# Performance work log

Hardware: AMD Instinct MI355X
Metric: run time of the kernel (lower is better)

The kernel has to match this reference:

```python
import jax, jax.numpy as jnp
import numpy as np
import math

N, C, H = 2048, 256, 8
D = C // H
T, R, E = 8, 12, 32768
BUCKETS = 21
SEED = 128


def _layernorm(x, g, b, eps=1e-5):
    mu = jnp.mean(x, axis=-1, keepdims=True)
    var = jnp.var(x, axis=-1, keepdims=True)
    return (x - mu) * jax.lax.rsqrt(var + eps) * g + b


def _bucketize_dt(dt, num_buckets):
    eps = 1e-06
    signed_log = jnp.sign(dt) * jnp.log1p(jnp.abs(dt) + eps)
    min_v, max_v = -5.0, 5.0
    norm = (jnp.clip(signed_log, min_v, max_v) - min_v) / (max_v - min_v + 1e-09)
    idx = jnp.floor(norm * (num_buckets - 1)).astype(jnp.int32)
    return jnp.clip(idx, 0, num_buckets - 1)


def setup_inputs() -> dict:
    key = jax.random.key(0)
    ks = jax.random.split(key, 24)
    s = 0.02
    inp = {
        'X': jax.random.normal(ks[0], (N, C), jnp.float32),
        'token_type': jax.random.randint(ks[1], (N,), 0, T, jnp.int32),
        'edge_src': jax.random.randint(ks[2], (E,), 0, N, jnp.int32),
        'edge_dst': jax.random.randint(ks[3], (E,), 0, N, jnp.int32),
        'edge_rel': jax.random.randint(ks[4], (E,), 0, R, jnp.int32),
        'time_vec': jax.random.normal(ks[5], (N,), jnp.float32),
        'seed_count': SEED,
        'Wq': jax.random.normal(ks[6], (C, C), jnp.float32) * s,
        'bq': jnp.zeros((C,), jnp.float32),
        'Wk': jax.random.normal(ks[7], (C, C), jnp.float32) * s,
        'bk': jnp.zeros((C,), jnp.float32),
        'Wv': jax.random.normal(ks[8], (C, C), jnp.float32) * s,
        'bv': jnp.zeros((C,), jnp.float32),
        'Wo': jax.random.normal(ks[9], (C, C), jnp.float32) * s,
        'bo': jnp.zeros((C,), jnp.float32),
        'ln1_g': jnp.ones((C,), jnp.float32),
        'ln1_b': jnp.zeros((C,), jnp.float32),
        'ln2_g': jnp.ones((C,), jnp.float32),
        'ln2_b': jnp.zeros((C,), jnp.float32),
        'W1': jax.random.normal(ks[10], (C, 4 * C), jnp.float32) * s,
        'b1': jnp.zeros((4 * C,), jnp.float32),
        'W2': jax.random.normal(ks[11], (4 * C, C), jnp.float32) * s,
        'b2': jnp.zeros((C,), jnp.float32),
        'adj_rel_bias': jnp.zeros((R, H), jnp.float32),
        'typepair_bias': jnp.zeros((T, T, H), jnp.float32),
        'temp_bias': jax.random.normal(ks[12], (BUCKETS, H), jnp.float32) * s,
    }
    return inp


def reference(X, token_type, edge_src, edge_dst, edge_rel, time_vec, seed_count,
              Wq, bq, Wk, bk, Wv, bv, Wo, bo,
              ln1_g, ln1_b, ln2_g, ln2_b, W1, b1, W2, b2,
              adj_rel_bias, typepair_bias, temp_bias):
    n = X.shape[0]
    h = _layernorm(X, ln1_g, ln1_b)
    q = (h @ Wq + bq).reshape(n, H, D)
    k = (h @ Wk + bk).reshape(n, H, D)
    v = (h @ Wv + bv).reshape(n, H, D)
    scores = jnp.einsum('nhd,mhd->hnm', q, k) / math.sqrt(D)  # [H, N, N]

    # structural bias, factored as [N, N, H] then transposed
    bias = typepair_bias[token_type][:, token_type]            # [N, N, H]
    bias = bias.at[edge_src, edge_dst].add(adj_rel_bias[edge_rel])
    # seed-wise temporal bias on the first seed_count rows
    dt = time_vec[None, :] - time_vec[:seed_count, None]       # [S, N]
    tb = temp_bias[_bucketize_dt(dt, BUCKETS)]                 # [S, N, H]
    bias = bias.at[:seed_count].add(tb)

    attn = jax.nn.softmax(scores + bias.transpose(2, 0, 1), axis=-1)
    o = jnp.einsum('hnm,mhd->nhd', attn, v).reshape(n, C)
    x = X + (o @ Wo + bo)

    h2 = _layernorm(x, ln2_g, ln2_b)
    f = jax.nn.gelu(h2 @ W1 + b1, approximate=False) @ W2 + b2
    return x + f
```

## Files before the change

### kernel.cpp

```cpp
#include <hip/hip_runtime.h>
#include <hip/hip_bf16.h>
#include <math.h>

#define NTOK 2048
#define CDIM 256
#define HHEADS 8
#define DHEAD 32
#define NEDGE 32768
#define EXTD 64
#define LE 72

typedef __attribute__((ext_vector_type(8))) short short8;
typedef __attribute__((ext_vector_type(4))) short short4v;
typedef __attribute__((ext_vector_type(4))) float f32x4;

static __device__ inline short f2bf(float f) {
    __hip_bfloat16 h = __float2bfloat16(f);
    return *reinterpret_cast<short*>(&h);
}
static __device__ inline float bf2f(short s) {
    unsigned int u = ((unsigned int)(unsigned short)s) << 16;
    return *reinterpret_cast<float*>(&u);
}

__global__ __launch_bounds__(256) void ln4_kernel(const float* __restrict__ X,
    const float* __restrict__ g, const float* __restrict__ b, short* __restrict__ out)
{
    int t = threadIdx.x;
    int wv = t >> 6, lane = t & 63;
    int row = blockIdx.x * 4 + wv;

    float4 x = *(const float4*)&X[(size_t)row * CDIM + lane * 4];
    float s = x.x + x.y + x.z + x.w;
    #pragma unroll
    for (int off = 1; off < 64; off <<= 1) s += __shfl_xor(s, off);
    float mu = s * (1.0f / CDIM);
    float4 d = { x.x - mu, x.y - mu, x.z - mu, x.w - mu };
    float s2 = d.x * d.x + d.y * d.y + d.z * d.z + d.w * d.w;
    #pragma unroll
    for (int off = 1; off < 64; off <<= 1) s2 += __shfl_xor(s2, off);
    float rsig = rsqrtf(s2 * (1.0f / CDIM) + 1e-5f);
    float4 gg = *(const float4*)&g[lane * 4];
    float4 bb = *(const float4*)&b[lane * 4];
    short o4[4];
    o4[0] = f2bf(d.x * rsig * gg.x + bb.x);
    o4[1] = f2bf(d.y * rsig * gg.y + bb.y);
    o4[2] = f2bf(d.z * rsig * gg.z + bb.z);
    o4[3] = f2bf(d.w * rsig * gg.w + bb.w);
    *(short4v*)&out[(size_t)row * CDIM + lane * 4] = *(short4v*)o4;
}

static __device__ inline void transpose_tile_f32(const float* __restrict__ in,
    short* __restrict__ out, int K, int N, int k0, int n0, int t)
{
    __shared__ float tile[64][65];
    int r0 = t >> 4, c0 = (t & 15) * 4;
    #pragma unroll
    for (int i = 0; i < 4; i++) {
        int r = r0 + i * 16;
        float4 v = *(const float4*)(in + (size_t)(k0 + r) * N + n0 + c0);
        tile[r][c0 + 0] = v.x; tile[r][c0 + 1] = v.y;
        tile[r][c0 + 2] = v.z; tile[r][c0 + 3] = v.w;
    }
    __syncthreads();
    #pragma unroll
    for (int i = 0; i < 4; i++) {
        int nr = r0 + i * 16;
        short o4[4];
        #pragma unroll
        for (int j = 0; j < 4; j++) o4[j] = f2bf(tile[c0 + j][nr]);
        *(short4v*)(out + (size_t)(n0 + nr) * K + k0 + c0) = *(short4v*)o4;
    }
}

__global__ __launch_bounds__(256) void prep_kernel(
    const float* __restrict__ Wq, const float* __restrict__ Wk,
    const float* __restrict__ Wv, const float* __restrict__ Wo,
    const float* __restrict__ W1, const float* __restrict__ W2,
    short* __restrict__ wt_qkv, short* __restrict__ wot,
    short* __restrict__ w1t, short* __restrict__ w2t,
    const int* __restrict__ token_type, const float* __restrict__ typepair_bias,
    short* __restrict__ qh, short* __restrict__ kh,
    int* __restrict__ cnt)
{
    int b = blockIdx.x;
    int t = threadIdx.x;
    if (b < 192) {
        const float* src; short* dst; int K, N, bx, by;
        if (b < 64) {
            int m = b >> 4, r = b & 15;
            src = (m == 0) ? Wq : (m == 1) ? Wk : (m == 2) ? Wv : Wo;
            dst = (m == 0) ? wt_qkv : (m == 1) ? wt_qkv + 256 * 256
                : (m == 2) ? wt_qkv + 512 * 256 : wot;
            K = 256; N = 256; bx = r & 3; by = r >> 2;
        } else if (b < 128) {
            int r = b - 64; src = W1; dst = w1t; K = 256; N = 1024; bx = r & 15; by = r >> 4;
        } else {
            int r = b - 128; src = W2; dst = w2t; K = 1024; N = 256; bx = r & 3; by = r >> 2;
        }
        transpose_tile_f32(src, dst, K, N, by * 64, bx * 64, t);
    } else if (b < 256) {
        int idx = (b - 192) * 256 + t;
        int row = idx >> 3, h = idx & 7;
        int tt = token_type[row];
        short qe[32], ke[32];
        #pragma unroll
        for (int j = 0; j < 32; j++) {
            if (j < 8) {
                qe[j] = f2bf(typepair_bias[(tt * 8 + j) * 8 + h]);
                ke[j] = (j == tt) ? (short)0x3F80 : (short)0;
            } else { qe[j] = 0; ke[j] = 0; }
        }
        size_t base = ((size_t)h * NTOK + row) * EXTD + 32;
        #pragma unroll
        for (int k = 0; k < 4; k++) {
            *(short8*)&qh[base + k * 8] = *(short8*)&qe[k * 8];
            *(short8*)&kh[base + k * 8] = *(short8*)&ke[k * 8];
        }
    } else {
        #pragma unroll
        for (int i = 0; i < 8; i++) cnt[t * 8 + i] = 0;
    }
}

template<int EPI>
__global__ __launch_bounds__(256) void gemm32_kernel(
    const short* __restrict__ A, const short* __restrict__ Bt,
    const float* __restrict__ bias, const float* __restrict__ resid,
    void* __restrict__ out_, int M, int N, int K)
{
    __shared__ short A_lds[32 * 40];
    __shared__ short B_lds[64 * 40];

    const int t = threadIdx.x;
    const int w = t >> 6, lane = t & 63, c = lane & 15, g = lane >> 4;
    const int row0 = blockIdx.y * 32, col0 = blockIdx.x * 64;
    const int srow = t >> 2, sk = (t & 3) * 8;

    f32x4 acc[2] = {};

    for (int k0 = 0; k0 < K; k0 += 32) {
        if (t < 128)
            *(short8*)&A_lds[srow * 40 + sk] = *(const short8*)&A[(size_t)(row0 + srow) * K + k0 + sk];
        *(short8*)&B_lds[srow * 40 + sk] = *(const short8*)&Bt[(size_t)(col0 + srow) * K + k0 + sk];
        __syncthreads();
        short8 af = *(const short8*)&A_lds[((w & 1) * 16 + c) * 40 + g * 8];
        #pragma unroll
        for (int nf = 0; nf < 2; nf++) {
            short8 bf = *(const short8*)&B_lds[((w >> 1) * 32 + nf * 16 + c) * 40 + g * 8];
            acc[nf] = __builtin_amdgcn_mfma_f32_16x16x32_bf16(af, bf, acc[nf], 0, 0, 0);
        }
        __syncthreads();
    }

    #pragma unroll
    for (int nf = 0; nf < 2; nf++) {
        #pragma unroll
        for (int reg = 0; reg < 4; reg++) {
            int row = row0 + (w & 1) * 16 + g * 4 + reg;
            int col = col0 + (w >> 1) * 32 + nf * 16 + c;
            float v = acc[nf][reg] + bias[col];
            if (EPI == 2) {
                ((float*)out_)[(size_t)row * N + col] = v + resid[(size_t)row * N + col];
            } else {
                v = 0.5f * v * (1.0f + erff(v * 0.70710678118654752f));
                ((short*)out_)[(size_t)row * N + col] = f2bf(v);
            }
        }
    }
}

__global__ __launch_bounds__(256) void gemm32_qkv_kernel(
    const short* __restrict__ A, const short* __restrict__ Bt,
    const float* __restrict__ bq, const float* __restrict__ bk, const float* __restrict__ bv,
    short* __restrict__ qh, short* __restrict__ kh, short* __restrict__ vt)
{
    const int K = CDIM;
    __shared__ short A_lds[32 * 40];
    __shared__ short B_lds[64 * 40];

    const int t = threadIdx.x;
    const int w = t >> 6, lane = t & 63, c = lane & 15, g = lane >> 4;
    const int row0 = blockIdx.y * 32, col0 = blockIdx.x * 64;
    const int srow = t >> 2, sk = (t & 3) * 8;

    f32x4 acc[2] = {};

    for (int k0 = 0; k0 < K; k0 += 32) {
        if (t < 128)
            *(short8*)&A_lds[srow * 40 + sk] = *(const short8*)&A[(size_t)(row0 + srow) * K + k0 + sk];
        *(short8*)&B_lds[srow * 40 + sk] = *(const short8*)&Bt[(size_t)(col0 + srow) * K + k0 + sk];
        __syncthreads();
        short8 af = *(const short8*)&A_lds[((w & 1) * 16 + c) * 40 + g * 8];
        #pragma unroll
        for (int nf = 0; nf < 2; nf++) {
            short8 bf = *(const short8*)&B_lds[((w >> 1) * 32 + nf * 16 + c) * 40 + g * 8];
            acc[nf] = __builtin_amdgcn_mfma_f32_16x16x32_bf16(af, bf, acc[nf], 0, 0, 0);
        }
        __syncthreads();
    }

    const int region = col0 >> 8;
    const int colr0 = col0 & 255;
    const float* bias = (region == 0) ? bq : (region == 1) ? bk : bv;
    #pragma unroll
    for (int nf = 0; nf < 2; nf++) {
        #pragma unroll
        for (int reg = 0; reg < 4; reg++) {
            int row = row0 + (w & 1) * 16 + g * 4 + reg;
            int col = colr0 + (w >> 1) * 32 + nf * 16 + c;
            float v = acc[nf][reg] + bias[col];
            if (region == 0) v *= 0.17677669529663687f;
            short bb = f2bf(v);
            size_t hidx = ((size_t)(col >> 5) * NTOK + row) * EXTD + (col & 31);
            if (region == 0)      qh[hidx] = bb;
            else if (region == 1) kh[hidx] = bb;
            else                  vt[(size_t)col * NTOK + row] = bb;
        }
    }
}

__global__ void edge_hist_kernel(const int* __restrict__ src, int* __restrict__ cnt, int E)
{
    int e = blockIdx.x * blockDim.x + threadIdx.x;
    if (e < E) atomicAdd(&cnt[src[e]], 1);
}

__global__ __launch_bounds__(256) void edge_scan_kernel(const int* __restrict__ cnt,
    int* __restrict__ row_ptr, int* __restrict__ wcur)
{
    __shared__ int sums[256];
    int t = threadIdx.x;
    int base = t * 8;
    int local[8];
    int s = 0;
    #pragma unroll
    for (int i = 0; i < 8; i++) { local[i] = s; s += cnt[base + i]; }
    sums[t] = s;
    __syncthreads();
    for (int off = 1; off < 256; off <<= 1) {
        int v = (t >= off) ? sums[t - off] : 0;
        __syncthreads();
        sums[t] += v;
        __syncthreads();
    }
    int excl = (t == 0) ? 0 : sums[t - 1];
    #pragma unroll
    for (int i = 0; i < 8; i++) {
        int r = excl + local[i];
        row_ptr[base + i] = r;
        wcur[base + i] = r;
    }
    if (t == 255) row_ptr[NTOK] = sums[255];
}

__global__ void edge_scatter_kernel(const int* __restrict__ src, const int* __restrict__ dst,
    const int* __restrict__ rel, int* __restrict__ wcur, int2* __restrict__ pairs, int E)
{
    int e = blockIdx.x * blockDim.x + threadIdx.x;
    if (e < E) {
        int pos = atomicAdd(&wcur[src[e]], 1);
        pairs[pos] = make_int2(dst[e], rel[e]);
    }
}

__global__ __launch_bounds__(256) void sgemm_kernel(
    const short* __restrict__ qh, const short* __restrict__ kh,
    short* __restrict__ S)
{
    __shared__ short A_lds[64 * LE];
    __shared__ short B_lds[64 * LE];
    const int t = threadIdx.x;
    const int w = t >> 6, lane = t & 63, c = lane & 15, g = lane >> 4;
    const int h = blockIdx.z;
    const int m0 = blockIdx.x * 64, n0 = blockIdx.y * 64;

    {
        int r = t >> 3, off = (t & 7) * 8;
        *(short8*)&A_lds[r * LE + off] =
            *(const short8*)&qh[((size_t)h * NTOK + n0 + r) * EXTD + off];
        *(short8*)&A_lds[(r + 32) * LE + off] =
            *(const short8*)&qh[((size_t)h * NTOK + n0 + 32 + r) * EXTD + off];
        *(short8*)&B_lds[r * LE + off] =
            *(const short8*)&kh[((size_t)h * NTOK + m0 + r) * EXTD + off];
        *(short8*)&B_lds[(r + 32) * LE + off] =
            *(const short8*)&kh[((size_t)h * NTOK + m0 + 32 + r) * EXTD + off];
    }
    __syncthreads();

    short8 alo = *(const short8*)&A_lds[(w * 16 + c) * LE + g * 8];
    short8 ahi = *(const short8*)&A_lds[(w * 16 + c) * LE + 32 + g * 8];
    f32x4 acc[4] = {};
    #pragma unroll
    for (int nf = 0; nf < 4; nf++) {
        short8 blo = *(const short8*)&B_lds[(nf * 16 + c) * LE + g * 8];
        short8 bhi = *(const short8*)&B_lds[(nf * 16 + c) * LE + 32 + g * 8];
        acc[nf] = __builtin_amdgcn_mfma_f32_16x16x32_bf16(alo, blo, acc[nf], 0, 0, 0);
        acc[nf] = __builtin_amdgcn_mfma_f32_16x16x32_bf16(ahi, bhi, acc[nf], 0, 0, 0);
    }

    #pragma unroll
    for (int nf = 0; nf < 4; nf++)
        #pragma unroll
        for (int reg = 0; reg < 4; reg++) {
            int row = n0 + w * 16 + g * 4 + reg;
            int col = m0 + nf * 16 + c;
            S[((size_t)h * NTOK + row) * NTOK + col] = f2bf(acc[nf][reg]);
        }
}

__global__ __launch_bounds__(256) void softmax_kernel(
    short* __restrict__ S,
    const float* __restrict__ time_vec, const int* __restrict__ seed_ptr,
    const float* __restrict__ adj_rel_bias, const float* __restrict__ temp_bias,
    const int* __restrict__ row_ptr, const int2* __restrict__ pairs)
{
    int t = threadIdx.x, wv = t >> 6, lane = t & 63;
    int task = blockIdx.x * 4 + wv;
    int h = task >> 11, n = task & 2047;
    int seed = seed_ptr[0];
    bool temporal = (n < seed);
    float tn = time_vec[n];
    short* Srow = &S[((size_t)h * NTOK + n) * NTOK];

    float vv[32];
    #pragma unroll
    for (int i = 0; i < 4; i++) {
        int m0 = i * 512 + lane * 8;
        short8 sv = *(const short8*)&Srow[m0];
        float v[8];
        #pragma unroll
        for (int j = 0; j < 8; j++) v[j] = bf2f(sv[j]);
        if (temporal) {
            float4 ta = *(const float4*)&time_vec[m0];
            float4 tb = *(const float4*)&time_vec[m0 + 4];
            float tv8[8] = { ta.x, ta.y, ta.z, ta.w, tb.x, tb.y, tb.z, tb.w };
            #pragma unroll
            for (int j = 0; j < 8; j++) {
                float dt = tv8[j] - tn;
                float ab = fabsf(dt) + 1e-6f;
                float sg = (dt > 0.0f) ? 1.0f : ((dt < 0.0f) ? -1.0f : 0.0f);
                float sl = sg * log1pf(ab);
                sl = fminf(fmaxf(sl, -5.0f), 5.0f);
                float norm = (sl + 5.0f) * (1.0f / (10.0f + 1e-9f));
                int bidx = (int)floorf(norm * 20.0f);
                bidx = min(max(bidx, 0), 20);
                v[j] += temp_bias[bidx * 8 + h];
            }
        }
        #pragma unroll
        for (int j = 0; j < 8; j++) vv[i * 8 + j] = v[j];
    }

    {
        int e0 = row_ptr[n], e1 = row_ptr[n + 1];
        for (int e = e0; e < e1; ++e) {
            int2 pr = pairs[e];
            int col = pr.x;
            if (((col >> 3) & 63) == lane) {
                float ab = adj_rel_bias[pr.y * 8 + h];
                int ci = col >> 9;
                int sl = col & 7;
                #pragma unroll
                for (int q = 0; q < 4; q++) {
                    if (q == ci) {
                        #pragma unroll
                        for (int j = 0; j < 8; j++)
                            vv[q * 8 + j] += (j == sl) ? ab : 0.0f;
                    }
                }
            }
        }
    }

    float mx = vv[0];
    #pragma unroll
    for (int i = 1; i < 32; i++) mx = fmaxf(mx, vv[i]);
    #pragma unroll
    for (int off = 1; off < 64; off <<= 1) mx = fmaxf(mx, __shfl_xor(mx, off));
    float sum = 0.0f;
    #pragma unroll
    for (int i = 0; i < 32; i++) { vv[i] = __expf(vv[i] - mx); sum += vv[i]; }
    #pragma unroll
    for (int off = 1; off < 64; off <<= 1) sum += __shfl_xor(sum, off);
    float inv = 1.0f / sum;

    #pragma unroll
    for (int i = 0; i < 4; i++) {
        short p8[8];
        #pragma unroll
        for (int j = 0; j < 8; j++) p8[j] = f2bf(vv[i * 8 + j] * inv);
        *(short8*)&Srow[i * 512 + lane * 8] = *(short8*)p8;
    }
}

__global__ __launch_bounds__(256) void pv_kernel(
    const short* __restrict__ P, const short* __restrict__ vt,
    short* __restrict__ o)
{
    __shared__ short A_lds[32 * LE];
    __shared__ short B_lds[32 * LE];
    const int t = threadIdx.x;
    const int w = t >> 6, lane = t & 63, c = lane & 15, g = lane >> 4;
    const int h = blockIdx.y;
    const int n0 = blockIdx.x * 32;
    const int rowblk = (w & 1) * 16, colblk = (w >> 1) * 16;

    f32x4 acc = {0.0f, 0.0f, 0.0f, 0.0f};

    for (int k0 = 0; k0 < NTOK; k0 += 64) {
        int r = t >> 3, off = (t & 7) * 8;
        *(short8*)&A_lds[r * LE + off] =
            *(const short8*)&P[((size_t)h * NTOK + n0 + r) * NTOK + k0 + off];
        *(short8*)&B_lds[r * LE + off] =
            *(const short8*)&vt[(size_t)(h * 32 + r) * NTOK + k0 + off];
        __syncthreads();
        short8 alo = *(const short8*)&A_lds[(rowblk + c) * LE + g * 8];
        short8 ahi = *(const short8*)&A_lds[(rowblk + c) * LE + 32 + g * 8];
        short8 blo = *(const short8*)&B_lds[(colblk + c) * LE + g * 8];
        short8 bhi = *(const short8*)&B_lds[(colblk + c) * LE + 32 + g * 8];
        acc = __builtin_amdgcn_mfma_f32_16x16x32_bf16(alo, blo, acc, 0, 0, 0);
        acc = __builtin_amdgcn_mfma_f32_16x16x32_bf16(ahi, bhi, acc, 0, 0, 0);
        __syncthreads();
    }

    #pragma unroll
    for (int reg = 0; reg < 4; reg++) {
        int row = n0 + rowblk + g * 4 + reg;
        int col = h * 32 + colblk + c;
        o[(size_t)row * CDIM + col] = f2bf(acc[reg]);
    }
}

extern "C" void kernel_launch(void* const* d_in, const int* in_sizes, int n_in,
                              void* d_out, int out_size, void* d_ws, size_t ws_size,
                              hipStream_t stream)
{
    (void)in_sizes; (void)n_in; (void)out_size; (void)ws_size;
    const float* X        = (const float*)d_in[0];
    const int* token_type = (const int*)d_in[1];
    const int* edge_src   = (const int*)d_in[2];
    const int* edge_dst   = (const int*)d_in[3];
    const int* edge_rel   = (const int*)d_in[4];
    const float* time_vec = (const float*)d_in[5];
    const int* seed_ptr   = (const int*)d_in[6];
    const float* Wq = (const float*)d_in[7];  const float* bq = (const float*)d_in[8];
    const float* Wk = (const float*)d_in[9];  const float* bk = (const float*)d_in[10];
    const float* Wv = (const float*)d_in[11]; const float* bv = (const float*)d_in[12];
    const float* Wo = (const float*)d_in[13]; const float* bo = (const float*)d_in[14];
    const float* ln1_g = (const float*)d_in[15]; const float* ln1_b = (const float*)d_in[16];
    const float* ln2_g = (const float*)d_in[17]; const float* ln2_b = (const float*)d_in[18];
    const float* W1 = (const float*)d_in[19]; const float* b1 = (const float*)d_in[20];
    const float* W2 = (const float*)d_in[21]; const float* b2 = (const float*)d_in[22];
    const float* adj_rel_bias  = (const float*)d_in[23];
    const float* typepair_bias = (const float*)d_in[24];
    const float* temp_bias     = (const float*)d_in[25];
    float* out = (float*)d_out;

    char* base = (char*)d_ws;
    size_t off = 0;
    auto alloc = [&](size_t bytes) { char* p = base + off; off += (bytes + 255) & ~(size_t)255; return p; };
    short* qh_bf   = (short*)alloc((size_t)HHEADS * NTOK * EXTD * 2);
    short* kh_bf   = (short*)alloc((size_t)HHEADS * NTOK * EXTD * 2);
    short* vt_bf   = (short*)alloc((size_t)256 * NTOK * 2);
    short* h1_bf   = (short*)alloc((size_t)NTOK * 256 * 2);
    short* h2_bf   = (short*)alloc((size_t)NTOK * 256 * 2);
    short* o_bf    = (short*)alloc((size_t)NTOK * 256 * 2);
    short* mid_bf  = (short*)alloc((size_t)NTOK * 1024 * 2);
    float* xb      = (float*)alloc((size_t)NTOK * 256 * 4);
    short* wt_qkv  = (short*)alloc((size_t)768 * 256 * 2);
    short* wot     = (short*)alloc((size_t)256 * 256 * 2);
    short* w1t     = (short*)alloc((size_t)1024 * 256 * 2);
    short* w2t     = (short*)alloc((size_t)256 * 1024 * 2);
    int2*  pairs   = (int2*)alloc((size_t)NEDGE * 8);
    int*   cnt     = (int*)alloc((size_t)NTOK * 4);
    int*   rowptr  = (int*)alloc(((size_t)NTOK + 1) * 4);
    int*   wcur    = (int*)alloc((size_t)NTOK * 4);
    short* S       = (short*)alloc((size_t)HHEADS * NTOK * NTOK * 2);

    prep_kernel<<<257, 256, 0, stream>>>(Wq, Wk, Wv, Wo, W1, W2,
                                         wt_qkv, wot, w1t, w2t,
                                         token_type, typepair_bias,
                                         qh_bf, kh_bf, cnt);

    edge_hist_kernel<<<NEDGE / 256, 256, 0, stream>>>(edge_src, cnt, NEDGE);
    edge_scan_kernel<<<1, 256, 0, stream>>>(cnt, rowptr, wcur);
    edge_scatter_kernel<<<NEDGE / 256, 256, 0, stream>>>(edge_src, edge_dst, edge_rel, wcur, pairs, NEDGE);

    ln4_kernel<<<NTOK / 4, 256, 0, stream>>>(X, ln1_g, ln1_b, h1_bf);

    gemm32_qkv_kernel<<<dim3(12, 64), 256, 0, stream>>>(h1_bf, wt_qkv, bq, bk, bv,
                                                        qh_bf, kh_bf, vt_bf);

    sgemm_kernel<<<dim3(32, 32, 8), 256, 0, stream>>>(qh_bf, kh_bf, S);
    softmax_kernel<<<NTOK * HHEADS / 4, 256, 0, stream>>>(
        S, time_vec, seed_ptr, adj_rel_bias, temp_bias, rowptr, pairs);
    pv_kernel<<<dim3(64, 8), 256, 0, stream>>>(S, vt_bf, o_bf);

    gemm32_kernel<2><<<dim3(4, 64), 256, 0, stream>>>(o_bf, wot, bo, X, xb, NTOK, 256, 256);

    ln4_kernel<<<NTOK / 4, 256, 0, stream>>>(xb, ln2_g, ln2_b, h2_bf);

    gemm32_kernel<3><<<dim3(16, 64), 256, 0, stream>>>(h2_bf, w1t, b1, nullptr, mid_bf, NTOK, 1024, 256);
    gemm32_kernel<2><<<dim3(4, 64), 256, 0, stream>>>(mid_bf, w2t, b2, xb, out, NTOK, 256, 1024);
}
```

Before: 155.5 us.

## Fuse bias and unnormalized exp into score GEMM, defer softmax normalization to PV

Folds the separate softmax pass into the QK^T GEMM epilogue: edge, temporal and type biases are added there, exp is taken without a max subtraction, and row sums are accumulated with atomics. Normalization moves into the PV epilogue. The edge CSR is rebuilt keyed by (row, 64-column tile) so each GEMM tile reads only its own edges. This removes a full read and write of the H×N×N score matrix, but it drops the max subtraction, which risks overflow for large scores, and adds atomic contention on the row sums.

```diff
diff --git a/kernel.cpp b/kernel.cpp
--- a/kernel.cpp
+++ b/kernel.cpp
@@ -7,6 +7,7 @@
 #define HHEADS 8
 #define DHEAD 32
 #define NEDGE 32768
+#define NTILE2 32
 #define EXTD 64
 #define LE 72
 
@@ -81,7 +82,7 @@
     short* __restrict__ w1t, short* __restrict__ w2t,
     const int* __restrict__ token_type, const float* __restrict__ typepair_bias,
     short* __restrict__ qh, short* __restrict__ kh,
-    int* __restrict__ cnt)
+    int* __restrict__ cnt2, float* __restrict__ rowsum)
 {
     int b = blockIdx.x;
     int t = threadIdx.x;
@@ -117,9 +118,14 @@
             *(short8*)&qh[base + k * 8] = *(short8*)&qe[k * 8];
             *(short8*)&kh[base + k * 8] = *(short8*)&ke[k * 8];
         }
+    } else if (b < 288) {
+        int base = (b - 256) * 2048 + t * 8;
+        #pragma unroll
+        for (int i = 0; i < 8; i++) cnt2[base + i] = 0;
     } else {
-        #pragma unroll
-        for (int i = 0; i < 8; i++) cnt[t * 8 + i] = 0;
+        int base = (b - 288) * 2048 + t * 8;
+        #pragma unroll
+        for (int i = 0; i < 8; i++) rowsum[base + i] = 0.0f;
     }
 }
 
@@ -220,22 +226,21 @@
     }
 }
 
-__global__ void edge_hist_kernel(const int* __restrict__ src, int* __restrict__ cnt, int E)
+__global__ void edge_hist2_kernel(const int* __restrict__ src, const int* __restrict__ dst,
+    int* __restrict__ cnt, int E)
 {
     int e = blockIdx.x * blockDim.x + threadIdx.x;
-    if (e < E) atomicAdd(&cnt[src[e]], 1);
-}
-
-__global__ __launch_bounds__(256) void edge_scan_kernel(const int* __restrict__ cnt,
+    if (e < E) atomicAdd(&cnt[src[e] * NTILE2 + (dst[e] >> 6)], 1);
+}
+
+__global__ __launch_bounds__(256) void edge_scan2_kernel(const int* __restrict__ cnt,
     int* __restrict__ row_ptr, int* __restrict__ wcur)
 {
     __shared__ int sums[256];
     int t = threadIdx.x;
-    int base = t * 8;
-    int local[8];
+    int base = t * 256;
     int s = 0;
-    #pragma unroll
-    for (int i = 0; i < 8; i++) { local[i] = s; s += cnt[base + i]; }
+    for (int i = 0; i < 256; i++) s += cnt[base + i];
     sums[t] = s;
     __syncthreads();
     for (int off = 1; off < 256; off <<= 1) {
@@ -244,36 +249,44 @@
         sums[t] += v;
         __syncthreads();
     }
-    int excl = (t == 0) ? 0 : sums[t - 1];
-    #pragma unroll
-    for (int i = 0; i < 8; i++) {
-        int r = excl + local[i];
-        row_ptr[base + i] = r;
-        wcur[base + i] = r;
-    }
-    if (t == 255) row_ptr[NTOK] = sums[255];
-}
-
-__global__ void edge_scatter_kernel(const int* __restrict__ src, const int* __restrict__ dst,
+    int run = (t == 0) ? 0 : sums[t - 1];
+    for (int i = 0; i < 256; i++) {
+        row_ptr[base + i] = run;
+        wcur[base + i] = run;
+        run += cnt[base + i];
+    }
+    if (t == 255) row_ptr[NTOK * NTILE2] = run;
+}
+
+__global__ void edge_scatter2_kernel(const int* __restrict__ src, const int* __restrict__ dst,
     const int* __restrict__ rel, int* __restrict__ wcur, int2* __restrict__ pairs, int E)
 {
     int e = blockIdx.x * blockDim.x + threadIdx.x;
     if (e < E) {
-        int pos = atomicAdd(&wcur[src[e]], 1);
-        pairs[pos] = make_int2(dst[e], rel[e]);
-    }
-}
-
-__global__ __launch_bounds__(256) void sgemm_kernel(
+        int d = dst[e];
+        int pos = atomicAdd(&wcur[src[e] * NTILE2 + (d >> 6)], 1);
+        pairs[pos] = make_int2(d, rel[e]);
+    }
+}
+
+__global__ __launch_bounds__(256) void sgemm_exp_kernel(
     const short* __restrict__ qh, const short* __restrict__ kh,
-    short* __restrict__ S)
+    const float* __restrict__ time_vec, const int* __restrict__ seed_ptr,
+    const float* __restrict__ adj_rel_bias, const float* __restrict__ temp_bias,
+    const int* __restrict__ row_ptr2, const int2* __restrict__ pairs2,
+    short* __restrict__ S, float* __restrict__ rowsum)
 {
     __shared__ short A_lds[64 * LE];
     __shared__ short B_lds[64 * LE];
+    __shared__ float tcol_s[64];
+    __shared__ float temp_h[21];
+    __shared__ float adj_h[12];
+
     const int t = threadIdx.x;
     const int w = t >> 6, lane = t & 63, c = lane & 15, g = lane >> 4;
     const int h = blockIdx.z;
     const int m0 = blockIdx.x * 64, n0 = blockIdx.y * 64;
+    const int seed = seed_ptr[0];
 
     {
         int r = t >> 3, off = (t & 7) * 8;
@@ -286,6 +299,9 @@
         *(short8*)&B_lds[(r + 32) * LE + off] =
             *(const short8*)&kh[((size_t)h * NTOK + m0 + 32 + r) * EXTD + off];
     }
+    if (t < 64) tcol_s[t] = time_vec[m0 + t];
+    if (t < 21) temp_h[t] = temp_bias[t * HHEADS + h];
+    if (t < 12) adj_h[t] = adj_rel_bias[t * HHEADS + h];
     __syncthreads();
 
     short8 alo = *(const short8*)&A_lds[(w * 16 + c) * LE + g * 8];
@@ -300,44 +316,35 @@
     }
 
     #pragma unroll
-    for (int nf = 0; nf < 4; nf++)
-        #pragma unroll
-        for (int reg = 0; reg < 4; reg++) {
-            int row = n0 + w * 16 + g * 4 + reg;
-            int col = m0 + nf * 16 + c;
-            S[((size_t)h * NTOK + row) * NTOK + col] = f2bf(acc[nf][reg]);
-        }
-}
-
-__global__ __launch_bounds__(256) void softmax_kernel(
-    short* __restrict__ S,
-    const float* __restrict__ time_vec, const int* __restrict__ seed_ptr,
-    const float* __restrict__ adj_rel_bias, const float* __restrict__ temp_bias,
-    const int* __restrict__ row_ptr, const int2* __restrict__ pairs)
-{
-    int t = threadIdx.x, wv = t >> 6, lane = t & 63;
-    int task = blockIdx.x * 4 + wv;
-    int h = task >> 11, n = task & 2047;
-    int seed = seed_ptr[0];
-    bool temporal = (n < seed);
-    float tn = time_vec[n];
-    short* Srow = &S[((size_t)h * NTOK + n) * NTOK];
-
-    float vv[32];
-    #pragma unroll
-    for (int i = 0; i < 4; i++) {
-        int m0 = i * 512 + lane * 8;
-        short8 sv = *(const short8*)&Srow[m0];
-        float v[8];
-        #pragma unroll
-        for (int j = 0; j < 8; j++) v[j] = bf2f(sv[j]);
-        if (temporal) {
-            float4 ta = *(const float4*)&time_vec[m0];
-            float4 tb = *(const float4*)&time_vec[m0 + 4];
-            float tv8[8] = { ta.x, ta.y, ta.z, ta.w, tb.x, tb.y, tb.z, tb.w };
-            #pragma unroll
-            for (int j = 0; j < 8; j++) {
-                float dt = tv8[j] - tn;
+    for (int reg = 0; reg < 4; reg++) {
+        const int rloc = w * 16 + g * 4 + reg;
+        const int n = n0 + rloc;
+        const bool rowTemp = (n < seed);
+        const float tn = time_vec[n];
+
+        {
+            int bidx = n * NTILE2 + (m0 >> 6);
+            int e0 = row_ptr2[bidx], e1 = row_ptr2[bidx + 1];
+            for (int e = e0; e < e1; ++e) {
+                int2 pr = pairs2[e];
+                int cl = pr.x & 63;
+                if ((cl & 15) == c) {
+                    float ab = adj_h[pr.y];
+                    int nfi = cl >> 4;
+                    #pragma unroll
+                    for (int nf = 0; nf < 4; nf++)
+                        if (nf == nfi) acc[nf][reg] += ab;
+                }
+            }
+        }
+
+        float rsum = 0.0f;
+        short p4[4];
+        #pragma unroll
+        for (int nf = 0; nf < 4; nf++) {
+            float s = acc[nf][reg];
+            if (rowTemp) {
+                float dt = tcol_s[nf * 16 + c] - tn;
                 float ab = fabsf(dt) + 1e-6f;
                 float sg = (dt > 0.0f) ? 1.0f : ((dt < 0.0f) ? -1.0f : 0.0f);
                 float sl = sg * log1pf(ab);
@@ -345,58 +352,26 @@
                 float norm = (sl + 5.0f) * (1.0f / (10.0f + 1e-9f));
                 int bidx = (int)floorf(norm * 20.0f);
                 bidx = min(max(bidx, 0), 20);
-                v[j] += temp_bias[bidx * 8 + h];
+                s += temp_h[bidx];
             }
-        }
-        #pragma unroll
-        for (int j = 0; j < 8; j++) vv[i * 8 + j] = v[j];
-    }
-
-    {
-        int e0 = row_ptr[n], e1 = row_ptr[n + 1];
-        for (int e = e0; e < e1; ++e) {
-            int2 pr = pairs[e];
-            int col = pr.x;
-            if (((col >> 3) & 63) == lane) {
-                float ab = adj_rel_bias[pr.y * 8 + h];
-                int ci = col >> 9;
-                int sl = col & 7;
-                #pragma unroll
-                for (int q = 0; q < 4; q++) {
-                    if (q == ci) {
-                        #pragma unroll
-                        for (int j = 0; j < 8; j++)
-                            vv[q * 8 + j] += (j == sl) ? ab : 0.0f;
-                    }
-                }
-            }
-        }
-    }
-
-    float mx = vv[0];
-    #pragma unroll
-    for (int i = 1; i < 32; i++) mx = fmaxf(mx, vv[i]);
-    #pragma unroll
-    for (int off = 1; off < 64; off <<= 1) mx = fmaxf(mx, __shfl_xor(mx, off));
-    float sum = 0.0f;
-    #pragma unroll
-    for (int i = 0; i < 32; i++) { vv[i] = __expf(vv[i] - mx); sum += vv[i]; }
-    #pragma unroll
-    for (int off = 1; off < 64; off <<= 1) sum += __shfl_xor(sum, off);
-    float inv = 1.0f / sum;
-
-    #pragma unroll
-    for (int i = 0; i < 4; i++) {
-        short p8[8];
-        #pragma unroll
-        for (int j = 0; j < 8; j++) p8[j] = f2bf(vv[i * 8 + j] * inv);
-        *(short8*)&Srow[i * 512 + lane * 8] = *(short8*)p8;
+            float e = __expf(s);
+            rsum += e;
+            p4[nf] = f2bf(e);
+        }
+        #pragma unroll
+        for (int nf = 0; nf < 4; nf++)
+            S[((size_t)h * NTOK + n) * NTOK + m0 + nf * 16 + c] = p4[nf];
+        rsum += __shfl_xor(rsum, 1);
+        rsum += __shfl_xor(rsum, 2);
+        rsum += __shfl_xor(rsum, 4);
+        rsum += __shfl_xor(rsum, 8);
+        if (c == 0) atomicAdd(&rowsum[h * NTOK + n], rsum);
     }
 }
 
 __global__ __launch_bounds__(256) void pv_kernel(
     const short* __restrict__ P, const short* __restrict__ vt,
-    short* __restrict__ o)
+    const float* __restrict__ rowsum, short* __restrict__ o)
 {
     __shared__ short A_lds[32 * LE];
     __shared__ short B_lds[32 * LE];
@@ -428,7 +403,8 @@
     for (int reg = 0; reg < 4; reg++) {
         int row = n0 + rowblk + g * 4 + reg;
         int col = h * 32 + colblk + c;
-        o[(size_t)row * CDIM + col] = f2bf(acc[reg]);
+        float inv = 1.0f / rowsum[h * NTOK + row];
+        o[(size_t)row * CDIM + col] = f2bf(acc[reg] * inv);
     }
 }
 
@@ -472,30 +448,31 @@
     short* wot     = (short*)alloc((size_t)256 * 256 * 2);
     short* w1t     = (short*)alloc((size_t)1024 * 256 * 2);
     short* w2t     = (short*)alloc((size_t)256 * 1024 * 2);
-    int2*  pairs   = (int2*)alloc((size_t)NEDGE * 8);
-    int*   cnt     = (int*)alloc((size_t)NTOK * 4);
-    int*   rowptr  = (int*)alloc(((size_t)NTOK + 1) * 4);
-    int*   wcur    = (int*)alloc((size_t)NTOK * 4);
+    int2*  pairs2  = (int2*)alloc((size_t)NEDGE * 8);
+    int*   cnt2    = (int*)alloc((size_t)NTOK * NTILE2 * 4);
+    int*   rowptr2 = (int*)alloc(((size_t)NTOK * NTILE2 + 1) * 4);
+    int*   wcur2   = (int*)alloc((size_t)NTOK * NTILE2 * 4);
+    float* rowsum  = (float*)alloc((size_t)HHEADS * NTOK * 4);
     short* S       = (short*)alloc((size_t)HHEADS * NTOK * NTOK * 2);
 
-    prep_kernel<<<257, 256, 0, stream>>>(Wq, Wk, Wv, Wo, W1, W2,
+    prep_kernel<<<296, 256, 0, stream>>>(Wq, Wk, Wv, Wo, W1, W2,
                                          wt_qkv, wot, w1t, w2t,
                                          token_type, typepair_bias,
-                                         qh_bf, kh_bf, cnt);
-
-    edge_hist_kernel<<<NEDGE / 256, 256, 0, stream>>>(edge_src, cnt, NEDGE);
-    edge_scan_kernel<<<1, 256, 0, stream>>>(cnt, rowptr, wcur);
-    edge_scatter_kernel<<<NEDGE / 256, 256, 0, stream>>>(edge_src, edge_dst, edge_rel, wcur, pairs, NEDGE);
+                                         qh_bf, kh_bf, cnt2, rowsum);
+
+    edge_hist2_kernel<<<NEDGE / 256, 256, 0, stream>>>(edge_src, edge_dst, cnt2, NEDGE);
+    edge_scan2_kernel<<<1, 256, 0, stream>>>(cnt2, rowptr2, wcur2);
+    edge_scatter2_kernel<<<NEDGE / 256, 256, 0, stream>>>(edge_src, edge_dst, edge_rel, wcur2, pairs2, NEDGE);
 
     ln4_kernel<<<NTOK / 4, 256, 0, stream>>>(X, ln1_g, ln1_b, h1_bf);
 
     gemm32_qkv_kernel<<<dim3(12, 64), 256, 0, stream>>>(h1_bf, wt_qkv, bq, bk, bv,
                                                         qh_bf, kh_bf, vt_bf);
 
-    sgemm_kernel<<<dim3(32, 32, 8), 256, 0, stream>>>(qh_bf, kh_bf, S);
-    softmax_kernel<<<NTOK * HHEADS / 4, 256, 0, stream>>>(
-        S, time_vec, seed_ptr, adj_rel_bias, temp_bias, rowptr, pairs);
-    pv_kernel<<<dim3(64, 8), 256, 0, stream>>>(S, vt_bf, o_bf);
+    sgemm_exp_kernel<<<dim3(32, 32, 8), 256, 0, stream>>>(
+        qh_bf, kh_bf, time_vec, seed_ptr, adj_rel_bias, temp_bias,
+        rowptr2, pairs2, S, rowsum);
+    pv_kernel<<<dim3(64, 8), 256, 0, stream>>>(S, vt_bf, rowsum, o_bf);
 
     gemm32_kernel<2><<<dim3(4, 64), 256, 0, stream>>>(o_bf, wot, bo, X, xb, NTOK, 256, 256);
 
```

After: 161.7 us. +4.0%, slower.
